# Kernel optimization log

Measured on AMD Instinct MI355X. Metric: run time of the kernel, lower is better.

## Reference

```python
import jax, jax.numpy as jnp
import numpy as np

K = 8                   # num_RQS_bins
MIN_BW = 1e-6; MIN_BH = 1e-6; MIN_D = 1e-6
TAIL = 12.0             # tail_bound for 'linear' tails
# binary masks for num_inputs=4: kept (conditioning) dims and transformed dims per layer
MASK_IDX = [(0, 2), (1, 3), (0, 1), (2, 3)]
INV_IDX = [(1, 3), (0, 2), (2, 3), (0, 1)]


def _rqs_forward(x, uw, uh, ud):
    """Unconstrained rational-quadratic spline, forward (direct) pass.
    x: [B,F]; uw,uh: [B,F,K]; ud: [B,F,K-1]. Returns (y, logabsdet) each [B,F]."""
    const = float(np.log(np.exp(1.0 - MIN_D) - 1.0))
    ud = jnp.pad(ud, ((0, 0), (0, 0), (1, 1)), constant_values=const)  # [B,F,K+1]
    inside = (x >= -TAIL) & (x <= TAIL)
    xc = jnp.clip(x, -TAIL, TAIL)

    widths = MIN_BW + (1.0 - MIN_BW * K) * jax.nn.softmax(uw, -1)
    cumw = jnp.pad(jnp.cumsum(widths, -1), ((0, 0), (0, 0), (1, 0)))
    cumw = 2.0 * TAIL * cumw - TAIL
    cumw = cumw.at[..., 0].set(-TAIL).at[..., -1].set(TAIL)
    widths = cumw[..., 1:] - cumw[..., :-1]

    heights = MIN_BH + (1.0 - MIN_BH * K) * jax.nn.softmax(uh, -1)
    cumh = jnp.pad(jnp.cumsum(heights, -1), ((0, 0), (0, 0), (1, 0)))
    cumh = 2.0 * TAIL * cumh - TAIL
    cumh = cumh.at[..., 0].set(-TAIL).at[..., -1].set(TAIL)
    heights = cumh[..., 1:] - cumh[..., :-1]

    derivs = MIN_D + jax.nn.softplus(ud)  # [B,F,K+1]

    # searchsorted over bin edges (forward mode uses cumwidths)
    idx = jnp.clip(jnp.sum((xc[..., None] >= cumw).astype(jnp.int32), -1) - 1, 0, K - 1)
    g = lambda t: jnp.take_along_axis(t, idx[..., None], axis=-1)[..., 0]
    in_cw, in_w = g(cumw), g(widths)
    in_ch, in_h = g(cumh), g(heights)
    delta = in_h / in_w
    d_k, d_k1 = g(derivs), g(derivs[..., 1:])

    theta = (xc - in_cw) / in_w
    tomt = theta * (1.0 - theta)
    num = in_h * (delta * theta ** 2 + d_k * tomt)
    den = delta + (d_k + d_k1 - 2.0 * delta) * tomt
    y = in_ch + num / den
    dnum = delta ** 2 * (d_k1 * theta ** 2 + 2.0 * delta * tomt + d_k * (1.0 - theta) ** 2)
    lad = jnp.log(dnum) - 2.0 * jnp.log(den)

    return jnp.where(inside, y, x), jnp.where(inside, lad, 0.0)


def setup_inputs() -> dict:
    key = jax.random.key(0)
    ks = jax.random.split(key, 5)
    B, H = 262144, 128
    OM = 3 * K - 1  # 23 params per transformed dim
    inputs = jax.random.normal(ks[0], (B, 4), jnp.float32)
    cond_inputs = jax.random.uniform(ks[1], (B, 1), jnp.float32)
    W1 = jax.random.normal(ks[2], (4, H, 3), jnp.float32) / np.sqrt(3.0)
    b1 = jnp.zeros((4, H), jnp.float32)
    W2 = jax.random.normal(ks[3], (4, H, H), jnp.float32) / np.sqrt(float(H))
    b2 = jnp.zeros((4, H), jnp.float32)
    W3 = jax.random.normal(ks[4], (4, 2 * OM, H), jnp.float32) / np.sqrt(float(H))
    b3 = jnp.zeros((4, 2 * OM), jnp.float32)
    return {"inputs": inputs, "cond_inputs": cond_inputs,
            "W1": W1, "b1": b1, "W2": W2, "b2": b2, "W3": W3, "b3": b3}


def reference(inputs, cond_inputs, W1, b1, W2, b2, W3, b3):
    B = inputs.shape[0]
    x = inputs
    logdets = jnp.zeros((B, 1), dtype=inputs.dtype)
    for l in range(4):  # fixed small number of coupling layers
        midx = list(MASK_IDX[l]); iidx = list(INV_IDX[l])
        m_in = jnp.concatenate([x[:, midx], cond_inputs], -1)  # [B,3]
        h = jax.nn.relu(m_in @ W1[l].T + b1[l])
        h = jax.nn.relu(h @ W2[l].T + b2[l])
        params = h @ W3[l].T + b3[l]  # [B, F*(3K-1)]
        F = len(iidx)
        tp = jnp.swapaxes(params.reshape(B, 3 * K - 1, F), 1, 2)  # [B,F,3K-1]
        y, lad = _rqs_forward(x[:, iidx], tp[..., :K], tp[..., K:2 * K], tp[..., 2 * K:])
        x = x.at[:, iidx].set(y)
        logdets = logdets + jnp.sum(lad, -1, keepdims=True)
    return x, logdets
```

## Files before the change

kernel.cpp:

```cpp
#include <hip/hip_runtime.h>

#define TAILB 12.0f
#define INV2048 4.8828125e-4f

typedef _Float16 half8 __attribute__((ext_vector_type(8)));
typedef _Float16 half4 __attribute__((ext_vector_type(4)));
typedef __fp16 fp16x2 __attribute__((ext_vector_type(2)));
typedef __attribute__((ext_vector_type(4))) float f32x4;

#define MFMAH __builtin_amdgcn_mfma_f32_16x16x32_f16

__device__ __forceinline__ float softplus_f(float z) {
    return (z > 15.f) ? z : __logf(1.f + __expf(z));
}

__device__ __forceinline__ void split2h(float v, _Float16& o0, _Float16& o1) {
    _Float16 h0 = (_Float16)v;
    float r1 = v - (float)h0;
    o0 = h0;
    o1 = (_Float16)(r1 * 2048.0f);
}

__device__ __forceinline__ void split4_pk(const float* v, half4& p0, half4& p1) {
    fp16x2 lo = __builtin_amdgcn_cvt_pkrtz(v[0], v[1]);
    fp16x2 hi = __builtin_amdgcn_cvt_pkrtz(v[2], v[3]);
    float r0 = (v[0] - (float)lo.x) * 2048.f;
    float r1 = (v[1] - (float)lo.y) * 2048.f;
    float r2 = (v[2] - (float)hi.x) * 2048.f;
    float r3 = (v[3] - (float)hi.y) * 2048.f;
    fp16x2 rlo = __builtin_amdgcn_cvt_pkrtz(r0, r1);
    fp16x2 rhi = __builtin_amdgcn_cvt_pkrtz(r2, r3);
    p0 = (half4){(_Float16)lo.x, (_Float16)lo.y, (_Float16)hi.x, (_Float16)hi.y};
    p1 = (half4){(_Float16)rlo.x, (_Float16)rlo.y, (_Float16)rhi.x, (_Float16)rhi.y};
}

__global__ __launch_bounds__(256)
void prep_v14(const float* __restrict__ W1, const float* __restrict__ b1,
              const float* __restrict__ W2, const float* __restrict__ W3,
              _Float16* __restrict__ W2F, _Float16* __restrict__ W3F,
              float4* __restrict__ w1p)
{
    int id = blockIdx.x * 256 + threadIdx.x;
    if (id < 65536) {
        int j = id & 7, ln = (id >> 3) & 63, tile = id >> 9;
        int cs = tile & 3, t = (tile >> 2) & 1, wv = (tile >> 3) & 3, l = tile >> 5;
        int n = 32 * wv + 16 * t + (ln & 15);
        int k = 32 * cs + 8 * (ln >> 4) + j;
        _Float16 a, b;
        split2h(W2[l * 16384 + n * 128 + k], a, b);
        W2F[(tile * 2 + 0) * 512 + ln * 8 + j] = a;
        W2F[(tile * 2 + 1) * 512 + ln * 8 + j] = b;
    } else if (id < 90112) {
        int t2 = id - 65536;
        int j = t2 & 7, ln = (t2 >> 3) & 63, tile3 = t2 >> 9;
        int cs = tile3 & 3, q = tile3 >> 2;
        int wv = q % 3, l = q / 3;
        int p = 16 * wv + (ln & 15);
        int n = 32 * cs + 8 * (ln >> 4) + j;
        float v = (p < 46) ? W3[l * 5888 + p * 128 + n] : 0.f;
        _Float16 a, b;
        split2h(v, a, b);
        W3F[(tile3 * 2 + 0) * 512 + ln * 8 + j] = a;
        W3F[(tile3 * 2 + 1) * 512 + ln * 8 + j] = b;
    } else if (id < 90624) {
        int t = id - 90112;
        int l = t >> 7, k = t & 127;
        float4 v;
        v.x = W1[l * 384 + k * 3 + 0];
        v.y = W1[l * 384 + k * 3 + 1];
        v.z = W1[l * 384 + k * 3 + 2];
        v.w = b1[l * 128 + k];
        w1p[t] = v;
    }
}

__global__ __launch_bounds__(256, 3)
void rqs_v14(const float* __restrict__ inp, const float* __restrict__ cond,
             const _Float16* __restrict__ W2F, const _Float16* __restrict__ W3F,
             const float4* __restrict__ w1p,
             const float* __restrict__ b2, const float* __restrict__ b3,
             float* __restrict__ out, int B)
{
    __shared__ __align__(16) _Float16 planes[2][32][128];
    __shared__ float xbuf[32][5];

    char* plw = (char*)&planes[0][0][0];
    const char* pl = plw;
    float* ladb = (float*)(plw + 6656);

    const int tid  = threadIdx.x;
    const int base = blockIdx.x * 32;
    const int wv   = tid >> 6;
    const int ln   = tid & 63;
    const int sm   = ln & 15;
    const int qd   = ln >> 4;
    const int s1   = tid & 31;
    const int kh   = tid >> 5;

    int rdaddr[2][4];
    #pragma unroll
    for (int st = 0; st < 2; ++st)
        #pragma unroll
        for (int cs = 0; cs < 4; ++cs)
            rdaddr[st][cs] = (16 * st + sm) * 256 + (((4 * cs + qd) ^ sm) << 4);
    int wra[2];
    #pragma unroll
    for (int gi = 0; gi < 2; ++gi)
        wra[gi] = s1 * 256 + (((2 * kh + gi) ^ (s1 & 15)) << 4);
    int ewa[2][2];
    #pragma unroll
    for (int t = 0; t < 2; ++t)
        #pragma unroll
        for (int st = 0; st < 2; ++st) {
            int g = 4 * wv + 2 * t + (qd >> 1);
            ewa[t][st] = (16 * st + sm) * 256 + ((g ^ sm) << 4) + ((qd & 1) << 3);
        }
    int pwa[2];
    #pragma unroll
    for (int st = 0; st < 2; ++st)
        pwa[st] = (16 * st + sm) * 208 + (16 * wv + 4 * qd) * 4;

    if (tid < 32) {
        float4 xi = reinterpret_cast<const float4*>(inp)[base + tid];
        xbuf[tid][0] = xi.x; xbuf[tid][1] = xi.y;
        xbuf[tid][2] = xi.z; xbuf[tid][3] = xi.w;
        xbuf[tid][4] = cond[base + tid];
    }
    float ladreg = 0.f;
    __syncthreads();

    #pragma unroll 1
    for (int l = 0; l < 4; ++l) {
        int mi0, mi1, ii0, ii1;
        switch (l) {
            case 0:  mi0 = 0; mi1 = 2; ii0 = 1; ii1 = 3; break;
            case 1:  mi0 = 1; mi1 = 3; ii0 = 0; ii1 = 2; break;
            case 2:  mi0 = 0; mi1 = 1; ii0 = 2; ii1 = 3; break;
            default: mi0 = 2; mi1 = 3; ii0 = 0; ii1 = 1; break;
        }

        {
            float m0 = xbuf[s1][mi0], m1 = xbuf[s1][mi1], cc = xbuf[s1][4];
            const float4* w1l = w1p + l * 128;
            #pragma unroll
            for (int gi = 0; gi < 2; ++gi) {
                int kb = (2 * kh + gi) * 8;
                float v[8];
                #pragma unroll
                for (int r = 0; r < 8; ++r) {
                    float4 w4 = w1l[kb + r];
                    v[r] = fmaxf(fmaf(w4.x, m0, fmaf(w4.y, m1, fmaf(w4.z, cc, w4.w))), 0.f);
                }
                half4 a0, a1, b0h, b1h;
                split4_pk(v, a0, a1);
                split4_pk(v + 4, b0h, b1h);
                half8 p0 = {a0.x, a0.y, a0.z, a0.w, b0h.x, b0h.y, b0h.z, b0h.w};
                half8 p1 = {a1.x, a1.y, a1.z, a1.w, b1h.x, b1h.y, b1h.z, b1h.w};
                char* wp = plw + wra[gi];
                *(half8*)(wp)        = p0;
                *(half8*)(wp + 8192) = p1;
            }
        }
        __syncthreads();

        f32x4 accA[2][2], accB[2][2];
        {
            int nb = __builtin_amdgcn_readfirstlane(l * 128 + 32 * wv);
            #pragma unroll
            for (int t = 0; t < 2; ++t) {
                float4 bias = *(const float4*)(b2 + nb + 16 * t + 4 * qd);
                #pragma unroll
                for (int st = 0; st < 2; ++st) {
                    accA[t][st] = (f32x4){bias.x, bias.y, bias.z, bias.w};
                    accB[t][st] = (f32x4){0.f, 0.f, 0.f, 0.f};
                }
            }
            const half8* W2F8 = (const half8*)W2F;
            int tb = (l * 4 + wv) * 2;
            #pragma unroll
            for (int cs = 0; cs < 4; ++cs) {
                half8 A00 = W2F8[(((tb + 0) * 4 + cs) * 2 + 0) * 64 + ln];
                half8 A01 = W2F8[(((tb + 0) * 4 + cs) * 2 + 1) * 64 + ln];
                half8 A10 = W2F8[(((tb + 1) * 4 + cs) * 2 + 0) * 64 + ln];
                half8 A11 = W2F8[(((tb + 1) * 4 + cs) * 2 + 1) * 64 + ln];
                #pragma unroll
                for (int st = 0; st < 2; ++st) {
                    half8 b0 = *(const half8*)(pl + rdaddr[st][cs]);
                    half8 b1 = *(const half8*)(pl + rdaddr[st][cs] + 8192);
                    accA[0][st] = MFMAH(A00, b0, accA[0][st], 0, 0, 0);
                    accB[0][st] = MFMAH(A00, b1, accB[0][st], 0, 0, 0);
                    accB[0][st] = MFMAH(A01, b0, accB[0][st], 0, 0, 0);
                    accA[1][st] = MFMAH(A10, b0, accA[1][st], 0, 0, 0);
                    accB[1][st] = MFMAH(A10, b1, accB[1][st], 0, 0, 0);
                    accB[1][st] = MFMAH(A11, b0, accB[1][st], 0, 0, 0);
                }
            }
        }
        __syncthreads();

        {
            #pragma unroll
            for (int t = 0; t < 2; ++t) {
                #pragma unroll
                for (int st = 0; st < 2; ++st) {
                    float v[4];
                    #pragma unroll
                    for (int r = 0; r < 4; ++r)
                        v[r] = fmaxf(fmaf(INV2048, accB[t][st][r], accA[t][st][r]), 0.f);
                    half4 p0, p1;
                    split4_pk(v, p0, p1);
                    char* wp = plw + ewa[t][st];
                    *(half4*)(wp)        = p0;
                    *(half4*)(wp + 8192) = p1;
                }
            }
        }
        __syncthreads();

        f32x4 acc3A[2], acc3B[2];
        #pragma unroll
        for (int st = 0; st < 2; ++st) {
            acc3A[st] = (f32x4){0.f, 0.f, 0.f, 0.f};
            acc3B[st] = (f32x4){0.f, 0.f, 0.f, 0.f};
        }
        if (wv < 3) {
            const half8* W3F8 = (const half8*)W3F;
            int qb = (l * 3 + wv) * 4;
            #pragma unroll
            for (int cs = 0; cs < 4; ++cs) {
                half8 A0 = W3F8[((qb + cs) * 2 + 0) * 64 + ln];
                half8 A1 = W3F8[((qb + cs) * 2 + 1) * 64 + ln];
                #pragma unroll
                for (int st = 0; st < 2; ++st) {
                    half8 b0 = *(const half8*)(pl + rdaddr[st][cs]);
                    half8 b1 = *(const half8*)(pl + rdaddr[st][cs] + 8192);
                    acc3A[st] = MFMAH(A0, b0, acc3A[st], 0, 0, 0);
                    acc3B[st] = MFMAH(A0, b1, acc3B[st], 0, 0, 0);
                    acc3B[st] = MFMAH(A1, b0, acc3B[st], 0, 0, 0);
                }
            }
        }
        __syncthreads();

        if (wv < 3) {
            #pragma unroll
            for (int st = 0; st < 2; ++st) {
                float4 pv;
                pv.x = fmaf(INV2048, acc3B[st][0], acc3A[st][0]);
                pv.y = fmaf(INV2048, acc3B[st][1], acc3A[st][1]);
                pv.z = fmaf(INV2048, acc3B[st][2], acc3A[st][2]);
                pv.w = fmaf(INV2048, acc3B[st][3], acc3A[st][3]);
                *(float4*)(plw + pwa[st]) = pv;
            }
        }
        __syncthreads();

        if (tid < 64) {
            int f = tid >> 5, s = tid & 31;
            const float* b3l = b3 + l * 46;
            const float4* prow = (const float4*)(pl + s * 208);
            float pr[23];
            #pragma unroll
            for (int i = 0; i < 12; ++i) {
                float4 q = prow[i];
                pr[2 * i] = (f ? q.y : q.x) + b3l[4 * i + f];
                if (2 * i + 1 < 23)
                    pr[2 * i + 1] = (f ? q.w : q.z) + b3l[4 * i + 2 + f];
            }

            float xin = xbuf[s][f == 0 ? ii0 : ii1];

            float d[9];
            d[0] = 1.f; d[8] = 1.f;
            #pragma unroll
            for (int k = 1; k < 8; ++k) d[k] = 1e-6f + softplus_f(pr[16 + k - 1]);

            bool inside = (xin >= -TAILB) && (xin <= TAILB);
            float xc = fminf(fmaxf(xin, -TAILB), TAILB);

            float mw = pr[0], mh = pr[8];
            #pragma unroll
            for (int k = 1; k < 8; ++k) { mw = fmaxf(mw, pr[k]); mh = fmaxf(mh, pr[8 + k]); }
            float ew[8], eh[8], swm = 0.f, shm = 0.f;
            #pragma unroll
            for (int k = 0; k < 8; ++k) {
                ew[k] = __expf(pr[k] - mw);     swm += ew[k];
                eh[k] = __expf(pr[8 + k] - mh); shm += eh[k];
            }
            const float c1 = 1.f - 8e-6f;
            float isw = __fdividef(c1, swm), ish = __fdividef(c1, shm);

            float cum_w = 0.f, cum_h = 0.f;
            float cwk = -TAILB, chk = -TAILB;
            float s_cw = -TAILB, s_w = 2.f * TAILB, s_ch = -TAILB, s_h = 2.f * TAILB;
            float s_d0 = 1.f, s_d1 = d[1];
            #pragma unroll
            for (int k = 0; k < 8; ++k) {
                cum_w += fmaf(ew[k], isw, 1e-6f);
                cum_h += fmaf(eh[k], ish, 1e-6f);
                float cwn = (k == 7) ? TAILB : fmaf(2.f * TAILB, cum_w, -TAILB);
                float chn = (k == 7) ? TAILB : fmaf(2.f * TAILB, cum_h, -TAILB);
                bool ge = (xc >= cwk);
                s_cw = ge ? cwk : s_cw;  s_w = ge ? (cwn - cwk) : s_w;
                s_ch = ge ? chk : s_ch;  s_h = ge ? (chn - chk) : s_h;
                s_d0 = ge ? d[k] : s_d0; s_d1 = ge ? d[k + 1] : s_d1;
                cwk = cwn; chk = chn;
            }

            float rw    = __fdividef(1.f, s_w);
            float th    = (xc - s_cw) * rw;
            float delta = s_h * rw;
            float omt   = 1.f - th;
            float tomt  = th * omt;
            float num   = s_h * fmaf(delta, th * th, s_d0 * tomt);
            float den   = fmaf(s_d0 + s_d1 - 2.f * delta, tomt, delta);
            float y     = s_ch + __fdividef(num, den);
            float dnum  = delta * delta * (s_d1 * th * th + 2.f * delta * tomt + s_d0 * omt * omt);
            float lad   = __logf(dnum) - 2.f * __logf(den);

            xbuf[s][f == 0 ? ii0 : ii1] = inside ? y : xin;
            ladreg += inside ? lad : 0.f;
        }
        __syncthreads();
    }

    if (tid < 64) ladb[tid] = ladreg;
    __syncthreads();
    if (tid < 32) {
        float4 xo;
        xo.x = xbuf[tid][0]; xo.y = xbuf[tid][1];
        xo.z = xbuf[tid][2]; xo.w = xbuf[tid][3];
        reinterpret_cast<float4*>(out)[base + tid] = xo;
        out[(size_t)B * 4 + base + tid] = ladb[tid] + ladb[tid + 32];
    }
}

extern "C" void kernel_launch(void* const* d_in, const int* in_sizes, int n_in,
                              void* d_out, int out_size, void* d_ws, size_t ws_size,
                              hipStream_t stream) {
    const float* inp  = (const float*)d_in[0];
    const float* cond = (const float*)d_in[1];
    const float* W1   = (const float*)d_in[2];
    const float* b1   = (const float*)d_in[3];
    const float* W2   = (const float*)d_in[4];
    const float* b2   = (const float*)d_in[5];
    const float* W3   = (const float*)d_in[6];
    const float* b3   = (const float*)d_in[7];
    float* out = (float*)d_out;
    int B = in_sizes[0] / 4;

    char* ws = (char*)d_ws;
    _Float16* W2F = (_Float16*)(ws);
    _Float16* W3F = (_Float16*)(ws + 262144);
    float4*   w1p = (float4*)(ws + 360448);

    hipLaunchKernelGGL(prep_v14, dim3(354), dim3(256), 0, stream,
                       W1, b1, W2, W3, W2F, W3F, w1p);
    hipLaunchKernelGGL(rqs_v14, dim3(B / 32), dim3(256), 0, stream,
                       inp, cond, W2F, W3F, w1p, b2, b3, out, B);
}
```

Baseline: 273.2 us.

## Process each 32-sample block with a single wave instead of four

The kernel moves from four cooperating waves per 32-sample block to one 64-lane wave that does all layer-1, MFMA layer-2 and layer-3 work itself. Block barriers become wave-local LDS waitcnt fences, and the B fragments are loaded from LDS once per stage into registers. The aim is to drop the frequent __syncthreads and the idle waves in the layer-3 and spline stages. In exchange each wave carries four times the MFMA and weight-load work serially, which raises register pressure and may reduce latency hiding.

Result: no change. 269.5 us (-1.4%).

```diff
diff --git a/kernel.cpp b/kernel.cpp
--- a/kernel.cpp
+++ b/kernel.cpp
@@ -9,6 +9,12 @@
 typedef __attribute__((ext_vector_type(4))) float f32x4;
 
 #define MFMAH __builtin_amdgcn_mfma_f32_16x16x32_f16
+
+#define WAVE_SYNC() do {                                  \
+    __builtin_amdgcn_sched_barrier(0);                    \
+    asm volatile("s_waitcnt lgkmcnt(0)" ::: "memory");    \
+    __builtin_amdgcn_sched_barrier(0);                    \
+} while (0)
 
 __device__ __forceinline__ float softplus_f(float z) {
     return (z > 15.f) ? z : __logf(1.f + __expf(z));
@@ -35,7 +41,7 @@
 }
 
 __global__ __launch_bounds__(256)
-void prep_v14(const float* __restrict__ W1, const float* __restrict__ b1,
+void prep_v15(const float* __restrict__ W1, const float* __restrict__ b1,
               const float* __restrict__ W2, const float* __restrict__ W3,
               _Float16* __restrict__ W2F, _Float16* __restrict__ W3F,
               float4* __restrict__ w1p)
@@ -74,8 +80,8 @@
     }
 }
 
-__global__ __launch_bounds__(256, 3)
-void rqs_v14(const float* __restrict__ inp, const float* __restrict__ cond,
+__global__ __launch_bounds__(64, 2)
+void rqs_v15(const float* __restrict__ inp, const float* __restrict__ cond,
              const _Float16* __restrict__ W2F, const _Float16* __restrict__ W3F,
              const float4* __restrict__ w1p,
              const float* __restrict__ b2, const float* __restrict__ b3,
@@ -86,16 +92,13 @@
 
     char* plw = (char*)&planes[0][0][0];
     const char* pl = plw;
-    float* ladb = (float*)(plw + 6656);
-
-    const int tid  = threadIdx.x;
+
+    const int ln   = threadIdx.x;
     const int base = blockIdx.x * 32;
-    const int wv   = tid >> 6;
-    const int ln   = tid & 63;
     const int sm   = ln & 15;
     const int qd   = ln >> 4;
-    const int s1   = tid & 31;
-    const int kh   = tid >> 5;
+    const int s1   = ln & 31;
+    const int hi   = ln >> 5;
 
     int rdaddr[2][4];
     #pragma unroll
@@ -103,31 +106,16 @@
         #pragma unroll
         for (int cs = 0; cs < 4; ++cs)
             rdaddr[st][cs] = (16 * st + sm) * 256 + (((4 * cs + qd) ^ sm) << 4);
-    int wra[2];
-    #pragma unroll
-    for (int gi = 0; gi < 2; ++gi)
-        wra[gi] = s1 * 256 + (((2 * kh + gi) ^ (s1 & 15)) << 4);
-    int ewa[2][2];
-    #pragma unroll
-    for (int t = 0; t < 2; ++t)
-        #pragma unroll
-        for (int st = 0; st < 2; ++st) {
-            int g = 4 * wv + 2 * t + (qd >> 1);
-            ewa[t][st] = (16 * st + sm) * 256 + ((g ^ sm) << 4) + ((qd & 1) << 3);
-        }
-    int pwa[2];
-    #pragma unroll
-    for (int st = 0; st < 2; ++st)
-        pwa[st] = (16 * st + sm) * 208 + (16 * wv + 4 * qd) * 4;
-
-    if (tid < 32) {
-        float4 xi = reinterpret_cast<const float4*>(inp)[base + tid];
-        xbuf[tid][0] = xi.x; xbuf[tid][1] = xi.y;
-        xbuf[tid][2] = xi.z; xbuf[tid][3] = xi.w;
-        xbuf[tid][4] = cond[base + tid];
+    const int wrb = s1 * 256 + hi * 8;
+
+    if (ln < 32) {
+        float4 xi = reinterpret_cast<const float4*>(inp)[base + ln];
+        xbuf[ln][0] = xi.x; xbuf[ln][1] = xi.y;
+        xbuf[ln][2] = xi.z; xbuf[ln][3] = xi.w;
+        xbuf[ln][4] = cond[base + ln];
     }
     float ladreg = 0.f;
-    __syncthreads();
+    WAVE_SYNC();
 
     #pragma unroll 1
     for (int l = 0; l < 4; ++l) {
@@ -142,133 +130,135 @@
         {
             float m0 = xbuf[s1][mi0], m1 = xbuf[s1][mi1], cc = xbuf[s1][4];
             const float4* w1l = w1p + l * 128;
-            #pragma unroll
-            for (int gi = 0; gi < 2; ++gi) {
-                int kb = (2 * kh + gi) * 8;
-                float v[8];
-                #pragma unroll
-                for (int r = 0; r < 8; ++r) {
-                    float4 w4 = w1l[kb + r];
-                    v[r] = fmaxf(fmaf(w4.x, m0, fmaf(w4.y, m1, fmaf(w4.z, cc, w4.w))), 0.f);
-                }
-                half4 a0, a1, b0h, b1h;
-                split4_pk(v, a0, a1);
-                split4_pk(v + 4, b0h, b1h);
-                half8 p0 = {a0.x, a0.y, a0.z, a0.w, b0h.x, b0h.y, b0h.z, b0h.w};
-                half8 p1 = {a1.x, a1.y, a1.z, a1.w, b1h.x, b1h.y, b1h.z, b1h.w};
-                char* wp = plw + wra[gi];
-                *(half8*)(wp)        = p0;
-                *(half8*)(wp + 8192) = p1;
-            }
-        }
-        __syncthreads();
-
-        f32x4 accA[2][2], accB[2][2];
-        {
-            int nb = __builtin_amdgcn_readfirstlane(l * 128 + 32 * wv);
-            #pragma unroll
-            for (int t = 0; t < 2; ++t) {
-                float4 bias = *(const float4*)(b2 + nb + 16 * t + 4 * qd);
+            #pragma unroll 4
+            for (int g = 0; g < 16; ++g) {
+                float v[4];
+                #pragma unroll
+                for (int j = 0; j < 4; ++j) {
+                    float4 w4 = w1l[g * 8 + hi * 4 + j];
+                    v[j] = fmaxf(fmaf(w4.x, m0, fmaf(w4.y, m1, fmaf(w4.z, cc, w4.w))), 0.f);
+                }
+                half4 p0, p1;
+                split4_pk(v, p0, p1);
+                char* wp = plw + wrb + ((g ^ sm) << 4);
+                *(half4*)(wp)        = p0;
+                *(half4*)(wp + 8192) = p1;
+            }
+        }
+        WAVE_SYNC();
+
+        half8 bf[2][4][2];
+        #pragma unroll
+        for (int st = 0; st < 2; ++st)
+            #pragma unroll
+            for (int cs = 0; cs < 4; ++cs) {
+                bf[st][cs][0] = *(const half8*)(pl + rdaddr[st][cs]);
+                bf[st][cs][1] = *(const half8*)(pl + rdaddr[st][cs] + 8192);
+            }
+        WAVE_SYNC();
+
+        const half8* W2F8 = (const half8*)W2F;
+        #pragma unroll 1
+        for (int np = 0; np < 4; ++np) {
+            f32x4 accA[2][2], accB[2][2];
+            #pragma unroll
+            for (int i = 0; i < 2; ++i) {
+                float4 bias = *(const float4*)(b2 + l * 128 + (2 * np + i) * 16 + 4 * qd);
                 #pragma unroll
                 for (int st = 0; st < 2; ++st) {
-                    accA[t][st] = (f32x4){bias.x, bias.y, bias.z, bias.w};
-                    accB[t][st] = (f32x4){0.f, 0.f, 0.f, 0.f};
-                }
-            }
-            const half8* W2F8 = (const half8*)W2F;
-            int tb = (l * 4 + wv) * 2;
+                    accA[i][st] = (f32x4){bias.x, bias.y, bias.z, bias.w};
+                    accB[i][st] = (f32x4){0.f, 0.f, 0.f, 0.f};
+                }
+            }
             #pragma unroll
             for (int cs = 0; cs < 4; ++cs) {
-                half8 A00 = W2F8[(((tb + 0) * 4 + cs) * 2 + 0) * 64 + ln];
-                half8 A01 = W2F8[(((tb + 0) * 4 + cs) * 2 + 1) * 64 + ln];
-                half8 A10 = W2F8[(((tb + 1) * 4 + cs) * 2 + 0) * 64 + ln];
-                half8 A11 = W2F8[(((tb + 1) * 4 + cs) * 2 + 1) * 64 + ln];
-                #pragma unroll
-                for (int st = 0; st < 2; ++st) {
-                    half8 b0 = *(const half8*)(pl + rdaddr[st][cs]);
-                    half8 b1 = *(const half8*)(pl + rdaddr[st][cs] + 8192);
-                    accA[0][st] = MFMAH(A00, b0, accA[0][st], 0, 0, 0);
-                    accB[0][st] = MFMAH(A00, b1, accB[0][st], 0, 0, 0);
-                    accB[0][st] = MFMAH(A01, b0, accB[0][st], 0, 0, 0);
-                    accA[1][st] = MFMAH(A10, b0, accA[1][st], 0, 0, 0);
-                    accB[1][st] = MFMAH(A10, b1, accB[1][st], 0, 0, 0);
-                    accB[1][st] = MFMAH(A11, b0, accB[1][st], 0, 0, 0);
-                }
-            }
-        }
-        __syncthreads();
-
-        {
-            #pragma unroll
-            for (int t = 0; t < 2; ++t) {
+                #pragma unroll
+                for (int i = 0; i < 2; ++i) {
+                    int tile = l * 8 + 2 * np + i;
+                    half8 A0 = W2F8[((tile * 4 + cs) * 2 + 0) * 64 + ln];
+                    half8 A1 = W2F8[((tile * 4 + cs) * 2 + 1) * 64 + ln];
+                    #pragma unroll
+                    for (int st = 0; st < 2; ++st) {
+                        accA[i][st] = MFMAH(A0, bf[st][cs][0], accA[i][st], 0, 0, 0);
+                        accB[i][st] = MFMAH(A0, bf[st][cs][1], accB[i][st], 0, 0, 0);
+                        accB[i][st] = MFMAH(A1, bf[st][cs][0], accB[i][st], 0, 0, 0);
+                    }
+                }
+            }
+            #pragma unroll
+            for (int i = 0; i < 2; ++i) {
+                int g = 2 * (2 * np + i) + (qd >> 1);
                 #pragma unroll
                 for (int st = 0; st < 2; ++st) {
                     float v[4];
                     #pragma unroll
                     for (int r = 0; r < 4; ++r)
-                        v[r] = fmaxf(fmaf(INV2048, accB[t][st][r], accA[t][st][r]), 0.f);
+                        v[r] = fmaxf(fmaf(INV2048, accB[i][st][r], accA[i][st][r]), 0.f);
                     half4 p0, p1;
                     split4_pk(v, p0, p1);
-                    char* wp = plw + ewa[t][st];
+                    char* wp = plw + (16 * st + sm) * 256 + ((g ^ sm) << 4) + ((qd & 1) << 3);
                     *(half4*)(wp)        = p0;
                     *(half4*)(wp + 8192) = p1;
                 }
             }
         }
-        __syncthreads();
-
-        f32x4 acc3A[2], acc3B[2];
+        WAVE_SYNC();
+
         #pragma unroll
-        for (int st = 0; st < 2; ++st) {
-            acc3A[st] = (f32x4){0.f, 0.f, 0.f, 0.f};
-            acc3B[st] = (f32x4){0.f, 0.f, 0.f, 0.f};
-        }
-        if (wv < 3) {
-            const half8* W3F8 = (const half8*)W3F;
-            int qb = (l * 3 + wv) * 4;
+        for (int st = 0; st < 2; ++st)
             #pragma unroll
             for (int cs = 0; cs < 4; ++cs) {
-                half8 A0 = W3F8[((qb + cs) * 2 + 0) * 64 + ln];
-                half8 A1 = W3F8[((qb + cs) * 2 + 1) * 64 + ln];
+                bf[st][cs][0] = *(const half8*)(pl + rdaddr[st][cs]);
+                bf[st][cs][1] = *(const half8*)(pl + rdaddr[st][cs] + 8192);
+            }
+        WAVE_SYNC();
+
+        const half8* W3F8 = (const half8*)W3F;
+        #pragma unroll 1
+        for (int pt = 0; pt < 3; ++pt) {
+            f32x4 a3A[2], a3B[2];
+            #pragma unroll
+            for (int st = 0; st < 2; ++st) {
+                a3A[st] = (f32x4){0.f, 0.f, 0.f, 0.f};
+                a3B[st] = (f32x4){0.f, 0.f, 0.f, 0.f};
+            }
+            #pragma unroll
+            for (int cs = 0; cs < 4; ++cs) {
+                int q = (l * 3 + pt) * 4 + cs;
+                half8 A0 = W3F8[(q * 2 + 0) * 64 + ln];
+                half8 A1 = W3F8[(q * 2 + 1) * 64 + ln];
                 #pragma unroll
                 for (int st = 0; st < 2; ++st) {
-                    half8 b0 = *(const half8*)(pl + rdaddr[st][cs]);
-                    half8 b1 = *(const half8*)(pl + rdaddr[st][cs] + 8192);
-                    acc3A[st] = MFMAH(A0, b0, acc3A[st], 0, 0, 0);
-                    acc3B[st] = MFMAH(A0, b1, acc3B[st], 0, 0, 0);
-                    acc3B[st] = MFMAH(A1, b0, acc3B[st], 0, 0, 0);
-                }
-            }
-        }
-        __syncthreads();
-
-        if (wv < 3) {
+                    a3A[st] = MFMAH(A0, bf[st][cs][0], a3A[st], 0, 0, 0);
+                    a3B[st] = MFMAH(A0, bf[st][cs][1], a3B[st], 0, 0, 0);
+                    a3B[st] = MFMAH(A1, bf[st][cs][0], a3B[st], 0, 0, 0);
+                }
+            }
             #pragma unroll
             for (int st = 0; st < 2; ++st) {
                 float4 pv;
-                pv.x = fmaf(INV2048, acc3B[st][0], acc3A[st][0]);
-                pv.y = fmaf(INV2048, acc3B[st][1], acc3A[st][1]);
-                pv.z = fmaf(INV2048, acc3B[st][2], acc3A[st][2]);
-                pv.w = fmaf(INV2048, acc3B[st][3], acc3A[st][3]);
-                *(float4*)(plw + pwa[st]) = pv;
-            }
-        }
-        __syncthreads();
-
-        if (tid < 64) {
-            int f = tid >> 5, s = tid & 31;
+                pv.x = fmaf(INV2048, a3B[st][0], a3A[st][0]);
+                pv.y = fmaf(INV2048, a3B[st][1], a3A[st][1]);
+                pv.z = fmaf(INV2048, a3B[st][2], a3A[st][2]);
+                pv.w = fmaf(INV2048, a3B[st][3], a3A[st][3]);
+                *(float4*)(plw + (16 * st + sm) * 208 + (16 * pt + 4 * qd) * 4) = pv;
+            }
+        }
+        WAVE_SYNC();
+
+        {
             const float* b3l = b3 + l * 46;
-            const float4* prow = (const float4*)(pl + s * 208);
+            const float4* prow = (const float4*)(pl + s1 * 208);
             float pr[23];
             #pragma unroll
             for (int i = 0; i < 12; ++i) {
                 float4 q = prow[i];
-                pr[2 * i] = (f ? q.y : q.x) + b3l[4 * i + f];
+                pr[2 * i] = (hi ? q.y : q.x) + b3l[4 * i + hi];
                 if (2 * i + 1 < 23)
-                    pr[2 * i + 1] = (f ? q.w : q.z) + b3l[4 * i + 2 + f];
-            }
-
-            float xin = xbuf[s][f == 0 ? ii0 : ii1];
+                    pr[2 * i + 1] = (hi ? q.w : q.z) + b3l[4 * i + 2 + hi];
+            }
+
+            float xin = xbuf[s1][hi == 0 ? ii0 : ii1];
 
             float d[9];
             d[0] = 1.f; d[8] = 1.f;
@@ -318,20 +308,19 @@
             float dnum  = delta * delta * (s_d1 * th * th + 2.f * delta * tomt + s_d0 * omt * omt);
             float lad   = __logf(dnum) - 2.f * __logf(den);
 
-            xbuf[s][f == 0 ? ii0 : ii1] = inside ? y : xin;
+            xbuf[s1][hi == 0 ? ii0 : ii1] = inside ? y : xin;
             ladreg += inside ? lad : 0.f;
         }
-        __syncthreads();
+        WAVE_SYNC();
     }
 
-    if (tid < 64) ladb[tid] = ladreg;
-    __syncthreads();
-    if (tid < 32) {
+    float lsum = ladreg + __shfl(ladreg, (ln + 32) & 63, 64);
+    if (ln < 32) {
         float4 xo;
-        xo.x = xbuf[tid][0]; xo.y = xbuf[tid][1];
-        xo.z = xbuf[tid][2]; xo.w = xbuf[tid][3];
-        reinterpret_cast<float4*>(out)[base + tid] = xo;
-        out[(size_t)B * 4 + base + tid] = ladb[tid] + ladb[tid + 32];
+        xo.x = xbuf[ln][0]; xo.y = xbuf[ln][1];
+        xo.z = xbuf[ln][2]; xo.w = xbuf[ln][3];
+        reinterpret_cast<float4*>(out)[base + ln] = xo;
+        out[(size_t)B * 4 + base + ln] = lsum;
     }
 }
 
@@ -354,8 +343,8 @@
     _Float16* W3F = (_Float16*)(ws + 262144);
     float4*   w1p = (float4*)(ws + 360448);
 
-    hipLaunchKernelGGL(prep_v14, dim3(354), dim3(256), 0, stream,
+    hipLaunchKernelGGL(prep_v15, dim3(354), dim3(256), 0, stream,
                        W1, b1, W2, W3, W2F, W3F, w1p);
-    hipLaunchKernelGGL(rqs_v14, dim3(B / 32), dim3(256), 0, stream,
+    hipLaunchKernelGGL(rqs_v15, dim3(B / 32), dim3(64), 0, stream,
                        inp, cond, W2F, W3F, w1p, b2, b3, out, B);
 }
```
